# Performance work log

Measured on AMD Instinct MI355X. Metric: run time of the kernel, lower is better.

## Reference

```python
import jax, jax.numpy as jnp
import numpy as np

B, S, D = 8, 4096, 64
NEG = 10000.0


def setup_inputs() -> dict:
    key = jax.random.key(0)
    k1, k2, k3, k4 = jax.random.split(key, 4)
    query = jax.random.normal(k1, (B, S, D), dtype=jnp.float32)
    k_ = jax.random.normal(k2, (B, S, D), dtype=jnp.float32)
    v_ = jax.random.normal(k3, (B, S, D), dtype=jnp.float32)
    # padding mask [B, Sk]: mostly valid, tail padded for some rows
    lens = jax.random.randint(k4, (B,), S // 2, S + 1)
    mask = jnp.arange(S)[None, :] < lens[:, None]
    return {"query": query, "key": k_, "value": v_, "mask": mask}


def reference(query, key, value, mask):
    d = query.shape[-1]
    scale = 1.0 / jnp.sqrt(jnp.asarray(d, dtype=query.dtype))
    # e: [B, Sq, Sk]
    e = jnp.einsum("bqd,bkd->bqk", query, key) * scale
    # causal (history_only) mask: key index > query index gets -10000
    q_idx = jnp.arange(query.shape[1])[:, None]
    k_idx = jnp.arange(key.shape[1])[None, :]
    e = e - NEG * (k_idx > q_idx).astype(e.dtype)[None, :, :]
    # padding mask [B, 1, Sk]
    e = e - NEG * (1.0 - mask.astype(e.dtype))[:, None, :]
    attention = jax.nn.softmax(e, axis=-1)
    return jnp.einsum("bqk,bkd->bqd", attention, value)
```

## Files before the change

### kernel.cpp

```cpp
#include <hip/hip_runtime.h>
#include <hip/hip_bf16.h>

#define B_N 8
#define S_N 4096
#define D_N 64
#define NQT 64
#define TILE_BYTES 8192
#define SLOT_BYTES 4352

typedef __attribute__((ext_vector_type(8))) short bf16x8;
typedef __attribute__((ext_vector_type(4))) float f32x4;
typedef __attribute__((ext_vector_type(16))) float f32x16;
typedef unsigned uint2v __attribute__((ext_vector_type(2)));
typedef unsigned uint4v __attribute__((ext_vector_type(4)));

__device__ __forceinline__ float fast_exp2(float x) {
#if __has_builtin(__builtin_amdgcn_exp2f)
  return __builtin_amdgcn_exp2f(x);
#else
  return exp2f(x);
#endif
}

__device__ __forceinline__ unsigned f2bf_u(float x) {
  __hip_bfloat16 h = __float2bfloat16(x);
  return (unsigned)__builtin_bit_cast(unsigned short, h);
}
__device__ __forceinline__ unsigned pack2(float a, float b) {
  return f2bf_u(a) | (f2bf_u(b) << 16);
}

__device__ __forceinline__ void pl32swap(unsigned& a, unsigned& b) {
#if __has_builtin(__builtin_amdgcn_permlane32_swap)
  uint2v r = __builtin_amdgcn_permlane32_swap(a, b, false, false);
  a = r[0];
  b = r[1];
#else
  asm volatile("v_permlane32_swap_b32 %0, %1" : "+v"(a), "+v"(b));
#endif
}
__device__ __forceinline__ float xhalf_sum(float x) {
  unsigned a = __builtin_bit_cast(unsigned, x), b = a;
  pl32swap(a, b);
  return __builtin_bit_cast(float, a) + __builtin_bit_cast(float, b);
}

__global__ void __launch_bounds__(256)
lens_kernel(const unsigned* __restrict__ mask, int* __restrict__ lens) {
  int b = blockIdx.x, tid = threadIdx.x;
  unsigned first = mask[0];
  int cnt = 0;
  if (first == 0x01010101u) {
    const unsigned char* m = ((const unsigned char*)mask) + (size_t)b * S_N;
    for (int i = tid; i < S_N; i += 256) cnt += (m[i] != 0);
  } else if (first == 0x3F800000u) {
    const float* m = ((const float*)mask) + (size_t)b * S_N;
    for (int i = tid; i < S_N; i += 256) cnt += (m[i] != 0.0f);
  } else {
    const int* m = ((const int*)mask) + (size_t)b * S_N;
    for (int i = tid; i < S_N; i += 256) cnt += (m[i] != 0);
  }
#pragma unroll
  for (int off = 32; off > 0; off >>= 1) cnt += __shfl_down(cnt, off);
  __shared__ int acc[4];
  if ((tid & 63) == 0) acc[tid >> 6] = cnt;
  __syncthreads();
  if (tid == 0) lens[b] = acc[0] + acc[1] + acc[2] + acc[3];
}

__global__ void __launch_bounds__(256)
prep_kernel(const float* __restrict__ K, const float* __restrict__ V,
            char* __restrict__ Ks, char* __restrict__ VTs) {
  __shared__ float vl[64][72];
  const int bt = blockIdx.x, tid = threadIdx.x;
  const float* Kt = K + (size_t)bt * 4096;
  const float* Vt = V + (size_t)bt * 4096;
  char* Ko = Ks + (size_t)bt * TILE_BYTES;
  char* Vo = VTs + (size_t)bt * TILE_BYTES;
#pragma unroll
  for (int i = 0; i < 2; ++i) {
    int c = tid + i * 256;
    int r = c >> 3, j = c & 7;
    f32x4 a = *(const f32x4*)(Kt + r * 64 + j * 8);
    f32x4 b4 = *(const f32x4*)(Kt + r * 64 + j * 8 + 4);
    union { bf16x8 v; unsigned u[4]; } pk;
    pk.u[0] = pack2(a[0], a[1]);   pk.u[1] = pack2(a[2], a[3]);
    pk.u[2] = pack2(b4[0], b4[1]); pk.u[3] = pack2(b4[2], b4[3]);
    *(bf16x8*)(Ko + ((r >> 5) * 4 + (j >> 1)) * 1024 + (j & 1) * 512 +
               (r & 31) * 16) = pk.v;
    f32x4 va = *(const f32x4*)(Vt + r * 64 + j * 8);
    f32x4 vb = *(const f32x4*)(Vt + r * 64 + j * 8 + 4);
#pragma unroll
    for (int e = 0; e < 4; ++e) vl[j * 8 + e][r] = va[e];
#pragma unroll
    for (int e = 0; e < 4; ++e) vl[j * 8 + 4 + e][r] = vb[e];
  }
  __syncthreads();
#pragma unroll
  for (int i = 0; i < 2; ++i) {
    int c = tid + i * 256;
    int d = c >> 3, j = c & 7;
    f32x4 fa = *(const f32x4*)(&vl[d][j * 8]);
    f32x4 fb = *(const f32x4*)(&vl[d][j * 8 + 4]);
    union { bf16x8 v; unsigned u[4]; } pk;
    pk.u[0] = pack2(fa[0], fa[1]); pk.u[1] = pack2(fa[2], fa[3]);
    pk.u[2] = pack2(fb[0], fb[1]); pk.u[3] = pack2(fb[2], fb[3]);
    *(bf16x8*)(Vo + ((d >> 5) * 4 + (j >> 1)) * 1024 + (j & 1) * 512 +
               (d & 31) * 16) = pk.v;
  }
}

__global__ void __launch_bounds__(256)
attn_kernel(const float* __restrict__ Qg, const char* __restrict__ Ks,
            const char* __restrict__ VTs, const int* __restrict__ lens,
            float* __restrict__ Og, char* __restrict__ parts,
            int M, int U) {
  const int tid = threadIdx.x;
  const int lane = tid & 63;
  const int w = tid >> 6;
  const int bid = blockIdx.x;
  const int b = bid & 7;
  const int u2 = (bid >> 3) * 4 + w;
  const int ws = u2 & 1;
  const int u = (U - 1) - (u2 >> 1);
  int a = 0;
  while ((M * (a + 1) * (a + 2)) / 2 <= u) ++a;
  const int v = u - (M * a * (a + 1)) / 2;
  const int qt = a * M + v / (a + 1);
  const int s = v - (v / (a + 1)) * (a + 1);
  const int kq = a + 1;

  const int q0 = qt * 64;
  const int len = lens[b];
  int nt = (len + 63) >> 6;
  if (qt + 1 < nt) nt = qt + 1;
  const int beg = s * M;
  int cnt = nt - beg;
  if (cnt > M) cnt = M;
  if (cnt < 0) cnt = 0;

  const int q31 = lane & 31;
  const int h = lane >> 5;
  const int qg = q0 + ws * 32 + q31;

  const char* Kb = Ks + (size_t)(b * NQT) * TILE_BYTES;
  const char* Vb = VTs + (size_t)(b * NQT) * TILE_BYTES;

  constexpr float CS = 0.125f * 1.4426950408889634f;
  bf16x8 qf[4];
#pragma unroll
  for (int c = 0; c < 4; ++c) {
    const float* src = Qg + ((size_t)(b * S_N) + qg) * D_N + c * 16 + h * 8;
    f32x4 aa = *(const f32x4*)src;
    f32x4 b4 = *(const f32x4*)(src + 4);
    union { bf16x8 v; unsigned u[4]; } pk;
    pk.u[0] = pack2(aa[0] * CS, aa[1] * CS);
    pk.u[1] = pack2(aa[2] * CS, aa[3] * CS);
    pk.u[2] = pack2(b4[0] * CS, b4[1] * CS);
    pk.u[3] = pack2(b4[2] * CS, b4[3] * CS);
    qf[c] = pk.v;
  }

  f32x16 ot0 = {}, ot1 = {};
  float l = 0.0f;

  for (int j = 0; j < cnt; ++j) {
    const int t = beg + j;
    bf16x8 f[8];
    const char* Kt = Kb + (size_t)t * TILE_BYTES + lane * 16;
#pragma unroll
    for (int c = 0; c < 8; ++c) f[c] = *(const bf16x8*)(Kt + c * 1024);

    f32x16 s0, s1;
#pragma unroll
    for (int i = 0; i < 16; ++i) { s0[i] = -8.0f; s1[i] = -8.0f; }
#pragma unroll
    for (int c = 0; c < 4; ++c) {
      s0 = __builtin_amdgcn_mfma_f32_32x32x16_bf16(f[c], qf[c], s0, 0, 0, 0);
      s1 = __builtin_amdgcn_mfma_f32_32x32x16_bf16(f[4 + c], qf[c], s1, 0, 0, 0);
    }

    const char* Vt2 = Vb + (size_t)t * TILE_BYTES + lane * 16;
#pragma unroll
    for (int c = 0; c < 8; ++c) f[c] = *(const bf16x8*)(Vt2 + c * 1024);

    const int kv0 = t * 64;
    if (t == qt || kv0 + 64 > len) {
#pragma unroll
      for (int g = 0; g < 4; ++g)
#pragma unroll
        for (int jj = 0; jj < 4; ++jj) {
          int kl = 8 * g + 4 * h + jj;
          if (kv0 + kl > qg || kv0 + kl >= len) s0[g * 4 + jj] = -10000.0f;
          if (kv0 + 32 + kl > qg || kv0 + 32 + kl >= len) s1[g * 4 + jj] = -10000.0f;
        }
    }

    float ps0 = 0.f, ps1 = 0.f, ps2 = 0.f, ps3 = 0.f;
#pragma unroll
    for (int g = 0; g < 4; ++g) {
      s0[4 * g + 0] = fast_exp2(s0[4 * g + 0]); ps0 += s0[4 * g + 0];
      s0[4 * g + 1] = fast_exp2(s0[4 * g + 1]); ps1 += s0[4 * g + 1];
      s0[4 * g + 2] = fast_exp2(s0[4 * g + 2]); ps2 += s0[4 * g + 2];
      s0[4 * g + 3] = fast_exp2(s0[4 * g + 3]); ps3 += s0[4 * g + 3];
      s1[4 * g + 0] = fast_exp2(s1[4 * g + 0]); ps0 += s1[4 * g + 0];
      s1[4 * g + 1] = fast_exp2(s1[4 * g + 1]); ps1 += s1[4 * g + 1];
      s1[4 * g + 2] = fast_exp2(s1[4 * g + 2]); ps2 += s1[4 * g + 2];
      s1[4 * g + 3] = fast_exp2(s1[4 * g + 3]); ps3 += s1[4 * g + 3];
    }
    l += xhalf_sum((ps0 + ps1) + (ps2 + ps3));

    unsigned opk0[4][2], opk1[4][2];
#pragma unroll
    for (int g = 0; g < 4; ++g) {
      opk0[g][0] = pack2(s0[4 * g + 0], s0[4 * g + 1]);
      opk0[g][1] = pack2(s0[4 * g + 2], s0[4 * g + 3]);
      opk1[g][0] = pack2(s1[4 * g + 0], s1[4 * g + 1]);
      opk1[g][1] = pack2(s1[4 * g + 2], s1[4 * g + 3]);
    }
    bf16x8 pb[4];
#pragma unroll
    for (int c = 0; c < 4; ++c) {
      const unsigned(*o)[2] = (c < 2) ? opk0 : opk1;
      const int g0 = 2 * (c & 1), g1 = g0 + 1;
      unsigned a0 = o[g0][0], b0 = o[g1][0];
      unsigned a1 = o[g0][1], b1 = o[g1][1];
      pl32swap(a0, b0);
      pl32swap(a1, b1);
      union { bf16x8 v; unsigned u[4]; } pk;
      pk.u[0] = a0; pk.u[1] = a1; pk.u[2] = b0; pk.u[3] = b1;
      pb[c] = pk.v;
    }

#pragma unroll
    for (int c = 0; c < 4; ++c) {
      ot0 = __builtin_amdgcn_mfma_f32_32x32x16_bf16(f[c], pb[c], ot0, 0, 0, 0);
      ot1 = __builtin_amdgcn_mfma_f32_32x32x16_bf16(f[4 + c], pb[c], ot1, 0, 0, 0);
    }
  }

  if (kq == 1) {
    float linv = 1.0f / l;
    float* orow = Og + ((size_t)(b * S_N) + qg) * D_N;
#pragma unroll
    for (int g = 0; g < 4; ++g) {
      f32x4 oa = {ot0[4 * g + 0] * linv, ot0[4 * g + 1] * linv,
                  ot0[4 * g + 2] * linv, ot0[4 * g + 3] * linv};
      *(f32x4*)(orow + 8 * g + 4 * h) = oa;
      f32x4 ob = {ot1[4 * g + 0] * linv, ot1[4 * g + 1] * linv,
                  ot1[4 * g + 2] * linv, ot1[4 * g + 3] * linv};
      *(f32x4*)(orow + 32 + 8 * g + 4 * h) = ob;
    }
  } else {
    char* slot = parts + (((size_t)b * U + u) * 2 + ws) * SLOT_BYTES;
    unsigned wv[16];
#pragma unroll
    for (int jj = 0; jj < 8; ++jj) {
      wv[jj] = pack2(ot0[2 * jj], ot0[2 * jj + 1]);
      wv[8 + jj] = pack2(ot1[2 * jj], ot1[2 * jj + 1]);
    }
    uint4v* dst = (uint4v*)(slot + lane * 64);
#pragma unroll
    for (int q4 = 0; q4 < 4; ++q4)
      dst[q4] = (uint4v){wv[4 * q4], wv[4 * q4 + 1], wv[4 * q4 + 2], wv[4 * q4 + 3]};
    *(float*)(slot + 4096 + lane * 4) = l;
  }
}

__global__ void __launch_bounds__(128)
merge_kernel(const char* __restrict__ parts, float* __restrict__ Og,
             int M, int U) {
  const int bid = blockIdx.x;
  const int b = bid & 7, qt = bid >> 3;
  const int a = qt / M;
  const int kq = a + 1;
  if (kq == 1) return;
  const int tid = threadIdx.x;
  const int ws = tid >> 6;
  const int lane = tid & 63;
  const int base_u = (M * a * (a + 1)) / 2 + (qt - a * M) * (a + 1);

  float acc[32];
#pragma unroll
  for (int i = 0; i < 32; ++i) acc[i] = 0.0f;
  float L = 0.0f;
  for (int s2 = 0; s2 < kq; ++s2) {
    const char* slot =
        parts + (((size_t)b * U + base_u + s2) * 2 + ws) * SLOT_BYTES;
    const uint4v* src = (const uint4v*)(slot + lane * 64);
#pragma unroll
    for (int q4 = 0; q4 < 4; ++q4) {
      uint4v wv = src[q4];
#pragma unroll
      for (int e = 0; e < 4; ++e) {
        unsigned uw = wv[e];
        acc[2 * (4 * q4 + e)] += __builtin_bit_cast(float, uw << 16);
        acc[2 * (4 * q4 + e) + 1] += __builtin_bit_cast(float, uw & 0xFFFF0000u);
      }
    }
    L += *(const float*)(slot + 4096 + lane * 4);
  }
  float linv = 1.0f / L;
  const int q31 = lane & 31;
  const int h = lane >> 5;
  float* orow = Og + ((size_t)(b * S_N) + qt * 64 + ws * 32 + q31) * D_N;
#pragma unroll
  for (int dt = 0; dt < 2; ++dt)
#pragma unroll
    for (int g = 0; g < 4; ++g) {
      f32x4 w = {acc[dt * 16 + 4 * g + 0] * linv, acc[dt * 16 + 4 * g + 1] * linv,
                 acc[dt * 16 + 4 * g + 2] * linv, acc[dt * 16 + 4 * g + 3] * linv};
      *(f32x4*)(orow + dt * 32 + 8 * g + 4 * h) = w;
    }
}

extern "C" void kernel_launch(void* const* d_in, const int* in_sizes, int n_in,
                              void* d_out, int out_size, void* d_ws, size_t ws_size,
                              hipStream_t stream) {
  const float* Qg = (const float*)d_in[0];
  const float* Kg = (const float*)d_in[1];
  const float* Vg = (const float*)d_in[2];
  const unsigned* mask = (const unsigned*)d_in[3];
  float* Og = (float*)d_out;

  int* lens = (int*)d_ws;
  char* Ks = (char*)d_ws + 4096;
  char* VTs = Ks + (size_t)B_N * NQT * TILE_BYTES;
  char* parts = VTs + (size_t)B_N * NQT * TILE_BYTES;

  int M = 8, U = 288;
  size_t need = 4096 + ((size_t)2 * B_N * NQT * TILE_BYTES) +
                (size_t)B_N * 288 * 2 * SLOT_BYTES;
  if (ws_size < need) { M = 64; U = 64; }

  lens_kernel<<<dim3(B_N), dim3(256), 0, stream>>>(mask, lens);
  prep_kernel<<<dim3(B_N * NQT), dim3(256), 0, stream>>>(Kg, Vg, Ks, VTs);
  attn_kernel<<<dim3(B_N * U / 2), dim3(256), 0, stream>>>(Qg, Ks, VTs, lens,
                                                           Og, parts, M, U);
  if (M == 8)
    merge_kernel<<<dim3(B_N * NQT), dim3(128), 0, stream>>>(parts, Og, M, U);
}
```

Before: 59.44 us.

## Split KV tiles into 32-key halves with register double-buffered prefetch

Restructures the attention inner loop to process each 64-key tile as two 32-key halves, with K and V fragments for the next half loaded into ping-pong register buffers while the current half computes. MFMA sections are wrapped in s_setprio raises, and launch bounds now request 3 blocks per SIMD-occupancy hint. The aim is to hide global load latency behind compute and improve occupancy by shrinking live register state, at the cost of more loop iterations, per-half mask logic and possible register pressure from the double buffers.

Measured after the change: 156.0 us. +162.4%, slower.

```diff
diff --git a/kernel.cpp b/kernel.cpp
--- a/kernel.cpp
+++ b/kernel.cpp
@@ -110,7 +110,7 @@
   }
 }
 
-__global__ void __launch_bounds__(256)
+__global__ void __launch_bounds__(256, 3)
 attn_kernel(const float* __restrict__ Qg, const char* __restrict__ Ks,
             const char* __restrict__ VTs, const int* __restrict__ lens,
             float* __restrict__ Og, char* __restrict__ parts,
@@ -163,80 +163,94 @@
 
   f32x16 ot0 = {}, ot1 = {};
   float l = 0.0f;
-
-  for (int j = 0; j < cnt; ++j) {
-    const int t = beg + j;
-    bf16x8 f[8];
-    const char* Kt = Kb + (size_t)t * TILE_BYTES + lane * 16;
-#pragma unroll
-    for (int c = 0; c < 8; ++c) f[c] = *(const bf16x8*)(Kt + c * 1024);
-
-    f32x16 s0, s1;
-#pragma unroll
-    for (int i = 0; i < 16; ++i) { s0[i] = -8.0f; s1[i] = -8.0f; }
-#pragma unroll
-    for (int c = 0; c < 4; ++c) {
-      s0 = __builtin_amdgcn_mfma_f32_32x32x16_bf16(f[c], qf[c], s0, 0, 0, 0);
-      s1 = __builtin_amdgcn_mfma_f32_32x32x16_bf16(f[4 + c], qf[c], s1, 0, 0, 0);
-    }
-
-    const char* Vt2 = Vb + (size_t)t * TILE_BYTES + lane * 16;
-#pragma unroll
-    for (int c = 0; c < 8; ++c) f[c] = *(const bf16x8*)(Vt2 + c * 1024);
-
-    const int kv0 = t * 64;
-    if (t == qt || kv0 + 64 > len) {
+  const int H = 2 * cnt;
+
+  auto load_half = [&](int hs, bf16x8(&kd)[4], bf16x8(&vd)[4])
+      __attribute__((always_inline)) {
+    const int t = beg + (hs >> 1);
+    const int half = hs & 1;
+    const char* Kt = Kb + (size_t)t * TILE_BYTES + half * 4096 + lane * 16;
+    const char* Vt = Vb + (size_t)t * TILE_BYTES + half * 2048 + lane * 16;
+#pragma unroll
+    for (int c = 0; c < 4; ++c) kd[c] = *(const bf16x8*)(Kt + c * 1024);
+    vd[0] = *(const bf16x8*)(Vt);
+    vd[1] = *(const bf16x8*)(Vt + 1024);
+    vd[2] = *(const bf16x8*)(Vt + 4096);
+    vd[3] = *(const bf16x8*)(Vt + 5120);
+  };
+
+  bf16x8 kA[4], vA4[4], kB[4], vB4[4];
+  if (H > 0) load_half(0, kA, vA4);
+
+  auto body = [&](bf16x8(&kc)[4], bf16x8(&vc)[4], bf16x8(&kn)[4],
+                  bf16x8(&vn)[4], int hs) __attribute__((always_inline)) {
+    const int t = beg + (hs >> 1);
+    const int half = hs & 1;
+
+    f32x16 sv;
+#pragma unroll
+    for (int i = 0; i < 16; ++i) sv[i] = -8.0f;
+    __builtin_amdgcn_s_setprio(1);
+#pragma unroll
+    for (int c = 0; c < 4; ++c)
+      sv = __builtin_amdgcn_mfma_f32_32x32x16_bf16(kc[c], qf[c], sv, 0, 0, 0);
+    __builtin_amdgcn_s_setprio(0);
+
+    if (hs + 1 < H) load_half(hs + 1, kn, vn);
+
+    const int kb0 = t * 64 + half * 32;
+    if (t == qt || t * 64 + 64 > len) {
 #pragma unroll
       for (int g = 0; g < 4; ++g)
 #pragma unroll
         for (int jj = 0; jj < 4; ++jj) {
-          int kl = 8 * g + 4 * h + jj;
-          if (kv0 + kl > qg || kv0 + kl >= len) s0[g * 4 + jj] = -10000.0f;
-          if (kv0 + 32 + kl > qg || kv0 + 32 + kl >= len) s1[g * 4 + jj] = -10000.0f;
+          int kg = kb0 + 8 * g + 4 * h + jj;
+          if (kg > qg || kg >= len) sv[g * 4 + jj] = -10000.0f;
         }
     }
 
     float ps0 = 0.f, ps1 = 0.f, ps2 = 0.f, ps3 = 0.f;
 #pragma unroll
     for (int g = 0; g < 4; ++g) {
-      s0[4 * g + 0] = fast_exp2(s0[4 * g + 0]); ps0 += s0[4 * g + 0];
-      s0[4 * g + 1] = fast_exp2(s0[4 * g + 1]); ps1 += s0[4 * g + 1];
-      s0[4 * g + 2] = fast_exp2(s0[4 * g + 2]); ps2 += s0[4 * g + 2];
-      s0[4 * g + 3] = fast_exp2(s0[4 * g + 3]); ps3 += s0[4 * g + 3];
-      s1[4 * g + 0] = fast_exp2(s1[4 * g + 0]); ps0 += s1[4 * g + 0];
-      s1[4 * g + 1] = fast_exp2(s1[4 * g + 1]); ps1 += s1[4 * g + 1];
-      s1[4 * g + 2] = fast_exp2(s1[4 * g + 2]); ps2 += s1[4 * g + 2];
-      s1[4 * g + 3] = fast_exp2(s1[4 * g + 3]); ps3 += s1[4 * g + 3];
+      sv[4 * g + 0] = fast_exp2(sv[4 * g + 0]); ps0 += sv[4 * g + 0];
+      sv[4 * g + 1] = fast_exp2(sv[4 * g + 1]); ps1 += sv[4 * g + 1];
+      sv[4 * g + 2] = fast_exp2(sv[4 * g + 2]); ps2 += sv[4 * g + 2];
+      sv[4 * g + 3] = fast_exp2(sv[4 * g + 3]); ps3 += sv[4 * g + 3];
     }
     l += xhalf_sum((ps0 + ps1) + (ps2 + ps3));
 
-    unsigned opk0[4][2], opk1[4][2];
+    unsigned opk[4][2];
 #pragma unroll
     for (int g = 0; g < 4; ++g) {
-      opk0[g][0] = pack2(s0[4 * g + 0], s0[4 * g + 1]);
-      opk0[g][1] = pack2(s0[4 * g + 2], s0[4 * g + 3]);
-      opk1[g][0] = pack2(s1[4 * g + 0], s1[4 * g + 1]);
-      opk1[g][1] = pack2(s1[4 * g + 2], s1[4 * g + 3]);
-    }
-    bf16x8 pb[4];
-#pragma unroll
-    for (int c = 0; c < 4; ++c) {
-      const unsigned(*o)[2] = (c < 2) ? opk0 : opk1;
-      const int g0 = 2 * (c & 1), g1 = g0 + 1;
-      unsigned a0 = o[g0][0], b0 = o[g1][0];
-      unsigned a1 = o[g0][1], b1 = o[g1][1];
+      opk[g][0] = pack2(sv[4 * g + 0], sv[4 * g + 1]);
+      opk[g][1] = pack2(sv[4 * g + 2], sv[4 * g + 3]);
+    }
+    bf16x8 pb2[2];
+#pragma unroll
+    for (int c2 = 0; c2 < 2; ++c2) {
+      const int g0 = 2 * c2, g1 = g0 + 1;
+      unsigned a0 = opk[g0][0], b0 = opk[g1][0];
+      unsigned a1 = opk[g0][1], b1 = opk[g1][1];
       pl32swap(a0, b0);
       pl32swap(a1, b1);
       union { bf16x8 v; unsigned u[4]; } pk;
       pk.u[0] = a0; pk.u[1] = a1; pk.u[2] = b0; pk.u[3] = b1;
-      pb[c] = pk.v;
-    }
-
-#pragma unroll
-    for (int c = 0; c < 4; ++c) {
-      ot0 = __builtin_amdgcn_mfma_f32_32x32x16_bf16(f[c], pb[c], ot0, 0, 0, 0);
-      ot1 = __builtin_amdgcn_mfma_f32_32x32x16_bf16(f[4 + c], pb[c], ot1, 0, 0, 0);
-    }
+      pb2[c2] = pk.v;
+    }
+
+    __builtin_amdgcn_s_setprio(1);
+    ot0 = __builtin_amdgcn_mfma_f32_32x32x16_bf16(vc[0], pb2[0], ot0, 0, 0, 0);
+    ot0 = __builtin_amdgcn_mfma_f32_32x32x16_bf16(vc[1], pb2[1], ot0, 0, 0, 0);
+    ot1 = __builtin_amdgcn_mfma_f32_32x32x16_bf16(vc[2], pb2[0], ot1, 0, 0, 0);
+    ot1 = __builtin_amdgcn_mfma_f32_32x32x16_bf16(vc[3], pb2[1], ot1, 0, 0, 0);
+    __builtin_amdgcn_s_setprio(0);
+  };
+
+  for (int hs = 0; hs < H; ++hs) {
+    if ((hs & 1) == 0)
+      body(kA, vA4, kB, vB4, hs);
+    else
+      body(kB, vB4, kA, vA4, hs);
   }
 
   if (kq == 1) {
```
